# Kernel optimization log

Hardware: AMD Instinct MI355X
Metric: run time of the kernel (lower is better)

## Reference

```python
import jax, jax.numpy as jnp
import numpy as np

B, D_IN, D_HID, NH, PF = 1024, 2048, 4096, 8, 2
D_UP = D_IN * PF          # 4096
HS = D_HID // NH          # 512 head size
EPS = 1e-5


def setup_inputs() -> dict:
    key = jax.random.key(0)
    ks = jax.random.split(key, 24)
    it = iter(range(24))

    def lin(k, fin, fout):
        # weight stored as (in, out); y = x @ W + b
        return jax.random.normal(k, (fin, fout), jnp.float32) / np.float32(np.sqrt(fin))

    def bd(k, fin_blk, fout_blk):
        # block-diagonal per-head weights (NH, in_blk, out_blk)
        return jax.random.normal(k, (NH, fin_blk, fout_blk), jnp.float32) / np.float32(np.sqrt(fin_blk))

    inp = {}
    inp['x'] = jax.random.normal(ks[next(it)], (B, D_IN), jnp.float32)
    inp['h_prev'] = jax.random.normal(ks[next(it)], (B, D_HID), jnp.float32)
    inp['c_prev'] = jax.random.normal(ks[next(it)], (B, D_HID), jnp.float32)
    inp['n_prev'] = jax.random.normal(ks[next(it)], (B, D_HID), jnp.float32)
    inp['m_prev'] = jax.random.normal(ks[next(it)], (B, D_HID), jnp.float32)
    inp['ln_w'] = jnp.ones((D_IN,), jnp.float32)
    inp['ln_b'] = jnp.zeros((D_IN,), jnp.float32)
    inp['upL_w'] = lin(ks[next(it)], D_IN, D_UP); inp['upL_b'] = jnp.zeros((D_UP,), jnp.float32)
    inp['upR_w'] = lin(ks[next(it)], D_IN, D_HID); inp['upR_b'] = jnp.zeros((D_HID,), jnp.float32)
    inp['conv_w'] = jax.random.normal(ks[next(it)], (1, 1, 4), jnp.float32) * 0.5  # (O,I,K)
    inp['conv_b'] = jnp.zeros((1,), jnp.float32)
    inp['skip_w'] = lin(ks[next(it)], D_UP, D_HID); inp['skip_b'] = jnp.zeros((D_HID,), jnp.float32)
    inp['wq'] = bd(ks[next(it)], D_UP // NH, HS); inp['bq'] = jnp.zeros((NH, HS), jnp.float32)
    inp['wk'] = bd(ks[next(it)], D_UP // NH, HS); inp['bk'] = jnp.zeros((NH, HS), jnp.float32)
    inp['wv'] = bd(ks[next(it)], D_UP // NH, HS); inp['bv'] = jnp.zeros((NH, HS), jnp.float32)
    inp['wi_w'] = lin(ks[next(it)], D_UP, D_HID); inp['wi_b'] = jnp.zeros((D_HID,), jnp.float32)
    inp['wf_w'] = lin(ks[next(it)], D_UP, D_HID); inp['wf_b'] = jnp.zeros((D_HID,), jnp.float32)
    inp['wo_w'] = lin(ks[next(it)], D_UP, D_HID); inp['wo_b'] = jnp.zeros((D_HID,), jnp.float32)
    inp['gn_w'] = jnp.ones((D_HID,), jnp.float32)
    inp['gn_b'] = jnp.zeros((D_HID,), jnp.float32)
    inp['down_w'] = lin(ks[next(it)], D_HID, D_IN); inp['down_b'] = jnp.zeros((D_IN,), jnp.float32)
    return inp


def _forward(x, h_prev, c_prev, n_prev, m_prev, ln_w, ln_b, upL_w, upL_b, upR_w, upR_b,
             conv_w, conv_b, skip_w, skip_b, wq, bq, wk, bk, wv, bv,
             wi_w, wi_b, wf_w, wf_b, wo_w, wo_b, gn_w, gn_b, down_w, down_b):
    b = x.shape[0]
    # LayerNorm(input_size)
    mu = jnp.mean(x, axis=-1, keepdims=True)
    var = jnp.var(x, axis=-1, keepdims=True)
    x_norm = (x - mu) * jax.lax.rsqrt(var + EPS) * ln_w + ln_b

    x_up_left = x_norm @ upL_w + upL_b     # (B, D_UP)
    x_up_right = x_norm @ upR_w + upR_b    # (B, D_HID)

    # CausalConv1D(1,1,4): left-pad 3, valid conv  == torch pad 3 both sides + drop last 3
    conv = jax.lax.conv_general_dilated(
        x_up_left[:, None, :], conv_w, window_strides=(1,), padding=((3, 0),),
        dimension_numbers=('NCH', 'OIH', 'NCH'))
    x_conv = jax.nn.silu(conv[:, 0, :] + conv_b[0])   # (B, D_UP)

    x_skip = x_conv @ skip_w + skip_b                 # (B, D_HID)

    def blockdiag(xv, w, bias):
        xh = xv.reshape(b, NH, -1)                    # (B, NH, in_blk)
        return (jnp.einsum('bhi,hio->bho', xh, w) + bias).reshape(b, -1)

    q = blockdiag(x_conv, wq, bq)                                  # (B, D_HID)
    k = blockdiag(x_conv, wk, bk) / np.float32(np.sqrt(HS))
    v = blockdiag(x_up_left, wv, bv)

    i_tilde = x_conv @ wi_w + wi_b
    f_tilde = x_conv @ wf_w + wf_b
    o = jax.nn.sigmoid(x_up_left @ wo_w + wo_b)

    # stabilized exponential gating
    m_t = jnp.maximum(f_tilde + m_prev, i_tilde)
    i_g = jnp.exp(i_tilde - m_t)
    f_g = jnp.exp(f_tilde + m_prev - m_t)
    c_t = f_g * c_prev + i_g * (v * k)
    n_t = f_g * n_prev + i_g * k

    # torch.max(torch.abs(n_t.T @ q), 1)[0] -> (D_HID,)
    denom = jnp.max(jnp.abs(n_t.T @ q), axis=1)
    h_t = o * (c_t * q) / denom                       # broadcast (B,D_HID)/(D_HID,)

    # GroupNorm(NH, D_HID) on 2D input
    hg = h_t.reshape(b, NH, HS)
    mu_g = jnp.mean(hg, axis=-1, keepdims=True)
    var_g = jnp.var(hg, axis=-1, keepdims=True)
    gn = ((hg - mu_g) * jax.lax.rsqrt(var_g + EPS)).reshape(b, D_HID) * gn_w + gn_b

    out = (gn + x_skip) * jax.nn.silu(x_up_right)
    final = out @ down_w + down_b + x
    return final, h_t, c_t, n_t, m_t


def reference(x, h_prev, c_prev, n_prev, m_prev, ln_w, ln_b, upL_w, upL_b, upR_w, upR_b,
              conv_w, conv_b, skip_w, skip_b, wq, bq, wk, bk, wv, bv,
              wi_w, wi_b, wf_w, wf_b, wo_w, wo_b, gn_w, gn_b, down_w, down_b):
    return _forward(x, h_prev, c_prev, n_prev, m_prev, ln_w, ln_b, upL_w, upL_b, upR_w, upR_b,
                    conv_w, conv_b, skip_w, skip_b, wq, bq, wk, bk, wv, bv,
                    wi_w, wi_b, wf_w, wf_b, wo_w, wo_b, gn_w, gn_b, down_w, down_b)
```

## Files before the change

### kernel.cpp

```cpp
#include <hip/hip_runtime.h>
#include <math.h>

#define B_ROWS 1024
#define D_IN   2048
#define D_HID  4096
#define D_UP   4096
#define NH     8
#define HS     512
#define LN_EPS 1e-5f

typedef __attribute__((ext_vector_type(8))) short bf16x8_t;
typedef __attribute__((ext_vector_type(4))) float f32x4_t;
typedef __attribute__((ext_vector_type(4))) unsigned short us4_t;

__device__ __forceinline__ unsigned short f2bf(float f) {
    unsigned int u = __float_as_uint(f);
    u += 0x7fffu + ((u >> 16) & 1u);
    return (unsigned short)(u >> 16);
}
__device__ __forceinline__ float bf2f(unsigned short u) {
    return __uint_as_float(((unsigned int)u) << 16);
}
__device__ __forceinline__ float sigmoidf_(float x) { return 1.0f / (1.0f + expf(-x)); }
__device__ __forceinline__ float siluf_(float x)    { return x / (1.0f + expf(-x)); }

__device__ __forceinline__ void gload16(const unsigned short* g, unsigned short* l) {
    __builtin_amdgcn_global_load_lds(
        (const __attribute__((address_space(1))) unsigned int*)(const void*)g,
        (__attribute__((address_space(3))) unsigned int*)(void*)l,
        16, 0, 0);
}

#define VMW(n) asm volatile("s_waitcnt vmcnt(" #n ")" ::: "memory")

#define XCD_SWZ()                                                        \
    int bx = blockIdx.x, by = blockIdx.y;                                \
    {                                                                    \
        const int gx_ = gridDim.x;                                       \
        const int n_  = gx_ * gridDim.y;                                 \
        if ((n_ & 7) == 0) {                                             \
            int lin = by * gx_ + bx;                                     \
            const int q8 = n_ >> 3;                                      \
            lin = (lin & 7) * q8 + (lin >> 3);                           \
            bx = lin % gx_; by = lin / gx_;                              \
        }                                                                \
    }

struct MGChunk {
    const unsigned short* A;
    const unsigned short* Bt;
    const float* bias;
    const float* resid;
    float* C;
    unsigned short* C2;
    float* denom;
    float alpha;
    int epi;
};

template<int NCH>
__global__ __launch_bounds__(256, 2) void mg256(
    MGChunk c0, MGChunk c1, MGChunk c2, MGChunk c3,
    int K, int lda, int ldbt, int ldc, int bpc,
    long aB, long wB, long bB, long cB)
{
    const int gx = gridDim.x, gy = gridDim.y;
    const int n = gx * gy;
    const int orig = blockIdx.y * gx + blockIdx.x;
    const int wl = ((n & 7) == 0) ? ((orig & 7) * (n >> 3) + (orig >> 3)) : orig;
    const int bxw = wl / gy;
    const int byw = wl - bxw * gy;
    const int chid = (NCH > 1) ? (bxw / bpc) : 0;
    const int cbx = bxw - chid * bpc;
    const MGChunk ch = (chid == 0) ? c0 : ((chid == 1) ? c1 : ((chid == 2) ? c2 : c3));
    const int bz = blockIdx.z;

    const unsigned short* A  = ch.A  + bz * aB;
    const unsigned short* Bt = ch.Bt + bz * wB;

    __shared__ __align__(16) unsigned short As[3][256][32];
    __shared__ __align__(16) unsigned short Bs[3][128][32];

    const int t = threadIdx.x;
    const int w = t >> 6, l = t & 63;
    const int wrm = w >> 1;
    const int wcn = w & 1;
    const long rowA = (long)byw * 256;
    const long rowB = (long)cbx * 128;

    const int skz = (((l & 3) ^ ((l >> 3) & 3)) << 3);
    const unsigned short* Ag = A  + rowA * (long)lda;
    const unsigned short* Bg = Bt + rowB * (long)ldbt;

    const int lm  = l & 15;
    const int pkz = (((l >> 4) ^ ((l >> 1) & 3)) << 3);

    f32x4_t acc[8][4];
#pragma unroll
    for (int mi = 0; mi < 8; ++mi)
#pragma unroll
        for (int ni = 0; ni < 4; ++ni) acc[mi][ni] = (f32x4_t)0.0f;

#define STAGE(buf, kb)                                                        \
    {                                                                         \
        _Pragma("unroll")                                                     \
        for (int p = 0; p < 4; ++p)                                           \
            gload16(Ag + (long)(w * 64 + p * 16 + (l >> 2)) * lda + (kb) + skz, \
                    &As[buf][w * 64 + p * 16][0]);                            \
        _Pragma("unroll")                                                     \
        for (int p = 0; p < 2; ++p)                                           \
            gload16(Bg + (long)(w * 32 + p * 16 + (l >> 2)) * ldbt + (kb) + skz, \
                    &Bs[buf][w * 32 + p * 16][0]);                            \
    }

    const int nsteps = K >> 5;
    STAGE(0, 0);
    STAGE(1, 32);

    int cur = 0;
    for (int ti = 0; ti < nsteps; ++ti) {
        int nxt2 = cur + 2; if (nxt2 >= 3) nxt2 -= 3;
        if (ti + 2 < nsteps) {
            STAGE(nxt2, (ti + 2) << 5);
            VMW(12);
        } else if (ti + 2 == nsteps) {
            VMW(6);
        } else {
            VMW(0);
        }
        __builtin_amdgcn_s_barrier();

        bf16x8_t bfr[4];
#pragma unroll
        for (int ni = 0; ni < 4; ++ni)
            bfr[ni] = *(const bf16x8_t*)&Bs[cur][wcn * 64 + ni * 16 + lm][pkz];
#pragma unroll
        for (int mi = 0; mi < 8; ++mi) {
            const bf16x8_t af = *(const bf16x8_t*)&As[cur][wrm * 128 + mi * 16 + lm][pkz];
#pragma unroll
            for (int ni = 0; ni < 4; ++ni)
                acc[mi][ni] = __builtin_amdgcn_mfma_f32_16x16x32_bf16(
                    af, bfr[ni], acc[mi][ni], 0, 0, 0);
        }

        asm volatile("s_waitcnt lgkmcnt(0)" ::: "memory");
        __builtin_amdgcn_s_barrier();
        cur = (cur == 2) ? 0 : cur + 1;
    }
#undef STAGE

    const int lr4 = (l >> 4) * 4;
    if (ch.epi == 3) {
        float rmax[8][4];
#pragma unroll
        for (int mi = 0; mi < 8; ++mi)
#pragma unroll
            for (int r = 0; r < 4; ++r) {
                float m = 0.0f;
#pragma unroll
                for (int ni = 0; ni < 4; ++ni) m = fmaxf(m, fabsf(acc[mi][ni][r]));
                rmax[mi][r] = m;
            }
#pragma unroll
        for (int off = 1; off < 16; off <<= 1)
#pragma unroll
            for (int mi = 0; mi < 8; ++mi)
#pragma unroll
                for (int r = 0; r < 4; ++r)
                    rmax[mi][r] = fmaxf(rmax[mi][r], __shfl_xor(rmax[mi][r], off, 64));
        if (lm == 0) {
#pragma unroll
            for (int mi = 0; mi < 8; ++mi)
#pragma unroll
                for (int r = 0; r < 4; ++r) {
                    const long m = rowA + wrm * 128 + mi * 16 + lr4 + r;
                    atomicMax((unsigned int*)&ch.denom[m], __float_as_uint(rmax[mi][r]));
                }
        }
        return;
    }
    const float* bias = ch.bias + bz * bB;
#pragma unroll
    for (int mi = 0; mi < 8; ++mi) {
        const long m0 = rowA + wrm * 128 + mi * 16 + lr4;
#pragma unroll
        for (int ni = 0; ni < 4; ++ni) {
            const long nn = rowB + wcn * 64 + ni * 16 + lm;
            const float bv = bias[nn];
#pragma unroll
            for (int r = 0; r < 4; ++r) {
                float v = acc[mi][ni][r] + bv;
                if (ch.epi == 2) v *= ch.alpha;
                const long m = m0 + r;
                if (ch.epi == 5) (ch.C2 + bz * cB)[m * ldc + nn] = f2bf(v);
                else             (ch.C  + bz * cB)[m * ldc + nn] = v;
            }
        }
    }
}

struct MCChunk {
    const unsigned short* A;
    const unsigned short* Bt;
    const float* bias;
    float* C;
    unsigned short* C2;
    float alpha;
    int epi;
};

template<int NCH>
__global__ __launch_bounds__(256) void mgemm_mc(
    MCChunk c0, MCChunk c1, MCChunk c2,
    int K, int lda, int ldbt, int ldc, int bpc,
    long aB, long wB, long bB, long cB)
{
    XCD_SWZ();
    const int chid = bx / bpc;
    const int cbx  = bx - chid * bpc;
    const MCChunk ch = (chid == 0) ? c0 : ((NCH > 1 && chid == 1) ? c1 : c2);
    const int bz = blockIdx.z;

    const unsigned short* A  = ch.A  + bz * aB;
    const unsigned short* Bt = ch.Bt + bz * wB;
    const float* bias = ch.bias + bz * bB;

    __shared__ __align__(16) unsigned short As[2][128][40];
    __shared__ __align__(16) unsigned short Bs[2][128][40];

    const int t = threadIdx.x;
    const int w = t >> 6, l = t & 63;
    const int wr = w >> 1, wc = w & 1;
    const long rowA = (long)by * 128;
    const long rowB = (long)cbx * 128;

    const int lr = t >> 2;
    const int lc = (t & 3) << 3;
    const unsigned short* Ag = A  + (rowA + lr) * (long)lda  + lc;
    const unsigned short* Bg = Bt + (rowB + lr) * (long)ldbt + lc;

    const int lm = l & 15;
    const int lk = (l >> 4) * 8;

    f32x4_t acc[4][4];
#pragma unroll
    for (int mi = 0; mi < 4; ++mi)
#pragma unroll
        for (int ni = 0; ni < 4; ++ni) acc[mi][ni] = (f32x4_t)0.0f;

    bf16x8_t ra[2], rb[2];
#pragma unroll
    for (int p = 0; p < 2; ++p) {
        ra[p] = *(const bf16x8_t*)(Ag + (long)p * 64 * lda);
        rb[p] = *(const bf16x8_t*)(Bg + (long)p * 64 * ldbt);
    }
#pragma unroll
    for (int p = 0; p < 2; ++p) {
        *(bf16x8_t*)&As[0][lr + p * 64][lc] = ra[p];
        *(bf16x8_t*)&Bs[0][lr + p * 64][lc] = rb[p];
    }
    __syncthreads();

    const int nsteps = K >> 5;
    for (int ti = 0; ti < nsteps; ++ti) {
        const int cur = ti & 1;
        if (ti + 1 < nsteps) {
            const int kb = (ti + 1) << 5;
#pragma unroll
            for (int p = 0; p < 2; ++p) {
                ra[p] = *(const bf16x8_t*)(Ag + (long)p * 64 * lda  + kb);
                rb[p] = *(const bf16x8_t*)(Bg + (long)p * 64 * ldbt + kb);
            }
        }
        bf16x8_t af[4], bfr[4];
#pragma unroll
        for (int mi = 0; mi < 4; ++mi)
            af[mi] = *(const bf16x8_t*)&As[cur][wr * 64 + mi * 16 + lm][lk];
#pragma unroll
        for (int ni = 0; ni < 4; ++ni)
            bfr[ni] = *(const bf16x8_t*)&Bs[cur][wc * 64 + ni * 16 + lm][lk];
#pragma unroll
        for (int mi = 0; mi < 4; ++mi)
#pragma unroll
            for (int ni = 0; ni < 4; ++ni)
                acc[mi][ni] = __builtin_amdgcn_mfma_f32_16x16x32_bf16(
                    af[mi], bfr[ni], acc[mi][ni], 0, 0, 0);
        if (ti + 1 < nsteps) {
            const int nxt = cur ^ 1;
#pragma unroll
            for (int p = 0; p < 2; ++p) {
                *(bf16x8_t*)&As[nxt][lr + p * 64][lc] = ra[p];
                *(bf16x8_t*)&Bs[nxt][lr + p * 64][lc] = rb[p];
            }
        }
        __syncthreads();
    }

    const int lr4 = (l >> 4) * 4;
    const float alpha = ch.alpha;
#pragma unroll
    for (int mi = 0; mi < 4; ++mi) {
        const long m0 = rowA + wr * 64 + mi * 16 + lr4;
#pragma unroll
        for (int ni = 0; ni < 4; ++ni) {
            const long nn = rowB + wc * 64 + ni * 16 + lm;
            const float bv = bias[nn];
#pragma unroll
            for (int r = 0; r < 4; ++r) {
                const float v = (acc[mi][ni][r] + bv) * alpha;
                const long m = m0 + r;
                if (ch.epi == 5) (ch.C2 + bz * cB)[m * ldc + nn] = f2bf(v);
                else             (ch.C  + bz * cB)[m * ldc + nn] = v;
            }
        }
    }
}

template<int BM, int EPI>
__global__ __launch_bounds__(256) void mgemm(
    const unsigned short* __restrict__ A, const unsigned short* __restrict__ Bt,
    const float* __restrict__ bias, const float* __restrict__ resid,
    float* __restrict__ C, float* __restrict__ denom,
    int K, int lda, int ldbt, int ldc)
{
    constexpr int MR = BM / 32;
    constexpr int AP = BM / 64;
    XCD_SWZ();

    __shared__ __align__(16) unsigned short As[2][BM][40];
    __shared__ __align__(16) unsigned short Bs[2][128][40];

    const int t = threadIdx.x;
    const int w = t >> 6, l = t & 63;
    const int wr = w >> 1, wc = w & 1;
    const long rowA = (long)by * BM;
    const long rowB = (long)bx * 128;

    const int lr = t >> 2;
    const int lc = (t & 3) << 3;
    const unsigned short* Ag = A  + (rowA + lr) * (long)lda  + lc;
    const unsigned short* Bg = Bt + (rowB + lr) * (long)ldbt + lc;

    const int lm = l & 15;
    const int lk = (l >> 4) * 8;

    f32x4_t acc[MR][4];
#pragma unroll
    for (int mi = 0; mi < MR; ++mi)
#pragma unroll
        for (int ni = 0; ni < 4; ++ni) acc[mi][ni] = (f32x4_t)0.0f;

    bf16x8_t ra[AP], rb[2];
#pragma unroll
    for (int p = 0; p < AP; ++p) ra[p] = *(const bf16x8_t*)(Ag + (long)p * 64 * lda);
#pragma unroll
    for (int p = 0; p < 2;  ++p) rb[p] = *(const bf16x8_t*)(Bg + (long)p * 64 * ldbt);
#pragma unroll
    for (int p = 0; p < AP; ++p) *(bf16x8_t*)&As[0][lr + p * 64][lc] = ra[p];
#pragma unroll
    for (int p = 0; p < 2;  ++p) *(bf16x8_t*)&Bs[0][lr + p * 64][lc] = rb[p];
    __syncthreads();

    const int nsteps = K >> 5;
    for (int ti = 0; ti < nsteps; ++ti) {
        const int cur = ti & 1;
        if (ti + 1 < nsteps) {
            const int kb = (ti + 1) << 5;
#pragma unroll
            for (int p = 0; p < AP; ++p) ra[p] = *(const bf16x8_t*)(Ag + (long)p * 64 * lda  + kb);
#pragma unroll
            for (int p = 0; p < 2;  ++p) rb[p] = *(const bf16x8_t*)(Bg + (long)p * 64 * ldbt + kb);
        }
        bf16x8_t af[MR], bfr[4];
#pragma unroll
        for (int mi = 0; mi < MR; ++mi)
            af[mi] = *(const bf16x8_t*)&As[cur][wr * (BM / 2) + mi * 16 + lm][lk];
#pragma unroll
        for (int ni = 0; ni < 4; ++ni)
            bfr[ni] = *(const bf16x8_t*)&Bs[cur][wc * 64 + ni * 16 + lm][lk];
#pragma unroll
        for (int mi = 0; mi < MR; ++mi)
#pragma unroll
            for (int ni = 0; ni < 4; ++ni)
                acc[mi][ni] = __builtin_amdgcn_mfma_f32_16x16x32_bf16(
                    af[mi], bfr[ni], acc[mi][ni], 0, 0, 0);
        if (ti + 1 < nsteps) {
            const int nxt = cur ^ 1;
#pragma unroll
            for (int p = 0; p < AP; ++p) *(bf16x8_t*)&As[nxt][lr + p * 64][lc] = ra[p];
#pragma unroll
            for (int p = 0; p < 2;  ++p) *(bf16x8_t*)&Bs[nxt][lr + p * 64][lc] = rb[p];
        }
        __syncthreads();
    }

    const int lr4 = (l >> 4) * 4;
#pragma unroll
    for (int mi = 0; mi < MR; ++mi) {
        const long m0 = rowA + wr * (BM / 2) + mi * 16 + lr4;
#pragma unroll
        for (int ni = 0; ni < 4; ++ni) {
            const long nn = rowB + wc * 64 + ni * 16 + lm;
            const float bv = bias[nn];
#pragma unroll
            for (int r = 0; r < 4; ++r) {
                float v = acc[mi][ni][r] + bv;
                const long m = m0 + r;
                if (EPI == 4) v += resid[m * ldc + nn];
                C[m * ldc + nn] = v;
            }
        }
    }
}

struct TP4 {
    const float* s0; const float* s1; const float* s2; const float* s3;
    unsigned short* d0; unsigned short* d1; unsigned short* d2; unsigned short* d3;
};

__global__ __launch_bounds__(256) void tp_batch(TP4 tp, int R, int C)
{
    const int z = blockIdx.z;
    const float* X = (z == 0) ? tp.s0 : (z == 1) ? tp.s1 : (z == 2) ? tp.s2 : tp.s3;
    unsigned short* XT = (z == 0) ? tp.d0 : (z == 1) ? tp.d1 : (z == 2) ? tp.d2 : tp.d3;
    __shared__ float tile[64][65];
    const int t = threadIdx.x;
    const long r0 = (long)blockIdx.y * 64;
    const long c0 = (long)blockIdx.x * 64;
    const int tr = t >> 4;
    const int tc = (t & 15) << 2;
#pragma unroll
    for (int p = 0; p < 4; ++p) {
        const float4 v = *(const float4*)(X + (r0 + tr + p * 16) * C + c0 + tc);
        tile[tr + p * 16][tc + 0] = v.x;
        tile[tr + p * 16][tc + 1] = v.y;
        tile[tr + p * 16][tc + 2] = v.z;
        tile[tr + p * 16][tc + 3] = v.w;
    }
    __syncthreads();
#pragma unroll
    for (int p = 0; p < 4; ++p) {
        const int cc = tr + p * 16;
        us4_t o;
        o.x = f2bf(tile[tc + 0][cc]);
        o.y = f2bf(tile[tc + 1][cc]);
        o.z = f2bf(tile[tc + 2][cc]);
        o.w = f2bf(tile[tc + 3][cc]);
        *(us4_t*)(XT + (c0 + cc) * (long)R + r0 + tc) = o;
    }
}

__global__ __launch_bounds__(256) void tp_qkv(
    const float* wq, const float* wk, const float* wv, unsigned short* dst)
{
    const int z = blockIdx.z;
    const int sel = z >> 3, head = z & 7;
    const float* X = ((sel == 0) ? wq : (sel == 1) ? wk : wv) + (long)head * HS * HS;
    unsigned short* XT = dst + (long)sel * NH * HS * HS + (long)head * HS * HS;
    __shared__ float tile[64][65];
    const int t = threadIdx.x;
    const long r0 = (long)blockIdx.y * 64;
    const long c0 = (long)blockIdx.x * 64;
    const int tr = t >> 4;
    const int tc = (t & 15) << 2;
#pragma unroll
    for (int p = 0; p < 4; ++p) {
        const float4 v = *(const float4*)(X + (r0 + tr + p * 16) * HS + c0 + tc);
        tile[tr + p * 16][tc + 0] = v.x;
        tile[tr + p * 16][tc + 1] = v.y;
        tile[tr + p * 16][tc + 2] = v.z;
        tile[tr + p * 16][tc + 3] = v.w;
    }
    __syncthreads();
#pragma unroll
    for (int p = 0; p < 4; ++p) {
        const int cc = tr + p * 16;
        us4_t o;
        o.x = f2bf(tile[tc + 0][cc]);
        o.y = f2bf(tile[tc + 1][cc]);
        o.z = f2bf(tile[tc + 2][cc]);
        o.w = f2bf(tile[tc + 3][cc]);
        *(us4_t*)(XT + (c0 + cc) * (long)HS + r0 + tc) = o;
    }
}

__global__ __launch_bounds__(256) void layernorm_kernel(
    const float* __restrict__ x, const float* __restrict__ w,
    const float* __restrict__ b, unsigned short* __restrict__ out)
{
    __shared__ float sh[8];
    const int row = blockIdx.x, t = threadIdx.x;
    const float* xr = x + (long)row * D_IN;
    float v[8];
    float s = 0.f, ss = 0.f;
#pragma unroll
    for (int i = 0; i < 8; ++i) {
        v[i] = xr[t + 256 * i];
        s += v[i];
        ss += v[i] * v[i];
    }
#pragma unroll
    for (int off = 32; off; off >>= 1) {
        s  += __shfl_down(s, off, 64);
        ss += __shfl_down(ss, off, 64);
    }
    const int lane = t & 63, wid = t >> 6;
    if (lane == 0) { sh[wid * 2] = s; sh[wid * 2 + 1] = ss; }
    __syncthreads();
    s = 0.f; ss = 0.f;
#pragma unroll
    for (int i = 0; i < 4; ++i) { s += sh[i * 2]; ss += sh[i * 2 + 1]; }
    const float mu  = s * (1.0f / D_IN);
    const float var = ss * (1.0f / D_IN) - mu * mu;
    const float rs  = rsqrtf(var + LN_EPS);
    unsigned short* orow = out + (long)row * D_IN;
#pragma unroll
    for (int i = 0; i < 8; ++i) {
        const int d = t + 256 * i;
        orow[d] = f2bf((v[i] - mu) * rs * w[d] + b[d]);
    }
}

__global__ void conv_silu_kernel(const unsigned short* __restrict__ xl,
                                 const float* __restrict__ cw,
                                 const float* __restrict__ cb,
                                 unsigned short* __restrict__ out)
{
    const long idx = (long)blockIdx.x * blockDim.x + threadIdx.x;
    if (idx >= (long)B_ROWS * D_UP) return;
    const int d = (int)(idx & (D_UP - 1));
    const float w0 = cw[0], w1 = cw[1], w2 = cw[2], w3 = cw[3];
    float acc = cb[0] + w3 * bf2f(xl[idx]);
    if (d >= 1) acc += w2 * bf2f(xl[idx - 1]);
    if (d >= 2) acc += w1 * bf2f(xl[idx - 2]);
    if (d >= 3) acc += w0 * bf2f(xl[idx - 3]);
    out[idx] = f2bf(siluf_(acc));
}

__global__ void gating_kernel(const float* __restrict__ it, const float* __restrict__ ft,
                              const float* __restrict__ mp, const float* __restrict__ cp,
                              const float* __restrict__ np_, const float* __restrict__ kk,
                              const float* __restrict__ vv,
                              float* __restrict__ mt, float* __restrict__ ct,
                              float* __restrict__ nt)
{
    const long idx = (long)blockIdx.x * blockDim.x + threadIdx.x;
    if (idx >= (long)B_ROWS * D_HID) return;
    const float i_t = it[idx];
    const float f_t = ft[idx] + mp[idx];
    const float m_t = fmaxf(f_t, i_t);
    const float i_g = expf(i_t - m_t);
    const float f_g = expf(f_t - m_t);
    const float kv  = kk[idx];
    ct[idx] = f_g * cp[idx] + i_g * (vv[idx] * kv);
    nt[idx] = f_g * np_[idx] + i_g * kv;
    mt[idx] = m_t;
}

__global__ __launch_bounds__(128) void hgnorm_kernel(
    const unsigned short* __restrict__ op, const float* __restrict__ ct,
    const float* __restrict__ qb, const float* __restrict__ denom,
    const float* __restrict__ gw, const float* __restrict__ gb,
    const unsigned short* __restrict__ xskip, const unsigned short* __restrict__ xupR,
    float* __restrict__ ht, unsigned short* __restrict__ out)
{
    __shared__ float sh[4];
    const int b = blockIdx.x >> 3, h = blockIdx.x & 7;
    const int t = threadIdx.x;
    const long base = (long)b * D_HID + h * HS;
    float v[4];
    float s = 0.f, ss = 0.f;
#pragma unroll
    for (int i = 0; i < 4; ++i) {
        const long ix = base + t + 128 * i;
        const int  dg = h * HS + t + 128 * i;
        const float hv = sigmoidf_(bf2f(op[ix])) * ct[ix] * qb[ix] / denom[dg];
        ht[ix] = hv;
        v[i] = hv;
        s += hv;
        ss += hv * hv;
    }
#pragma unroll
    for (int off = 32; off; off >>= 1) {
        s  += __shfl_down(s, off, 64);
        ss += __shfl_down(ss, off, 64);
    }
    if ((t & 63) == 0) { sh[(t >> 6) * 2] = s; sh[(t >> 6) * 2 + 1] = ss; }
    __syncthreads();
    s = sh[0] + sh[2];
    ss = sh[1] + sh[3];
    const float mu  = s * (1.0f / HS);
    const float var = ss * (1.0f / HS) - mu * mu;
    const float rs  = rsqrtf(var + LN_EPS);
#pragma unroll
    for (int i = 0; i < 4; ++i) {
        const int  dg = h * HS + t + 128 * i;
        const long ix = base + t + 128 * i;
        const float g = (v[i] - mu) * rs * gw[dg] + gb[dg];
        out[ix] = f2bf((g + bf2f(xskip[ix])) * siluf_(bf2f(xupR[ix])));
    }
}

extern "C" void kernel_launch(void* const* d_in, const int* in_sizes, int n_in,
                              void* d_out, int out_size, void* d_ws, size_t ws_size,
                              hipStream_t stream)
{
    const float* x      = (const float*)d_in[0];
    const float* c_prev = (const float*)d_in[2];
    const float* n_prev = (const float*)d_in[3];
    const float* m_prev = (const float*)d_in[4];
    const float* ln_w   = (const float*)d_in[5];
    const float* ln_b   = (const float*)d_in[6];
    const float* upL_w  = (const float*)d_in[7];
    const float* upL_b  = (const float*)d_in[8];
    const float* upR_w  = (const float*)d_in[9];
    const float* upR_b  = (const float*)d_in[10];
    const float* conv_w = (const float*)d_in[11];
    const float* conv_b = (const float*)d_in[12];
    const float* skip_w = (const float*)d_in[13];
    const float* skip_b = (const float*)d_in[14];
    const float* wq     = (const float*)d_in[15];
    const float* bq     = (const float*)d_in[16];
    const float* wk     = (const float*)d_in[17];
    const float* bk     = (const float*)d_in[18];
    const float* wv     = (const float*)d_in[19];
    const float* bv     = (const float*)d_in[20];
    const float* wi_w   = (const float*)d_in[21];
    const float* wi_b   = (const float*)d_in[22];
    const float* wf_w   = (const float*)d_in[23];
    const float* wf_b   = (const float*)d_in[24];
    const float* wo_w   = (const float*)d_in[25];
    const float* wo_b   = (const float*)d_in[26];
    const float* gn_w   = (const float*)d_in[27];
    const float* gn_b   = (const float*)d_in[28];
    const float* down_w = (const float*)d_in[29];
    const float* down_b = (const float*)d_in[30];

    float* out     = (float*)d_out;
    float* final_o = out;
    float* ht      = final_o + 2097152;
    float* ct      = ht + 4194304;
    float* nt      = ct + 4194304;
    float* mt      = nt + 4194304;

    unsigned short* WTA = (unsigned short*)ht;
    unsigned short* WTB = (unsigned short*)nt;

    const long M = 1048576;
    float* ws = (float*)d_ws;
    float* qb  = ws +  0 * M;
    float* kb  = ws +  4 * M;
    float* vb  = ws +  8 * M;
    float* itb = ws + 12 * M;
    float* ftb = ws + 16 * M;
    unsigned short* xupR_bf  = (unsigned short*)(ws + 20 * M);
    unsigned short* xskip_bf = (unsigned short*)(ws + 22 * M);
    unsigned short* opb_bf   = (unsigned short*)(ws + 24 * M);
    unsigned short* xnorm_bf = (unsigned short*)(ws + 26 * M);
    unsigned short* xupL_bf  = (unsigned short*)(ws + 27 * M);
    unsigned short* xconv_bf = (unsigned short*)(ws + 29 * M);
    float* denom             = ws + 31 * M;
    unsigned short* WTC      = (unsigned short*)(ws + 32 * M);
    unsigned short* WTD      = (unsigned short*)(ws +  0 * M);
    unsigned short* ntT      = (unsigned short*)(ws + 26 * M);
    unsigned short* qT       = (unsigned short*)(ws + 28 * M);
    unsigned short* dwT      = (unsigned short*)(ws + 12 * M);
    unsigned short* tmp_bf   = (unsigned short*)(ws +  8 * M);

    const float kscale = 1.0f / sqrtf((float)HS);
    const long HS2 = (long)HS * HS;
    MGChunk cz = {};
    MCChunk mz = {};

    layernorm_kernel<<<B_ROWS, 256, 0, stream>>>(x, ln_w, ln_b, xnorm_bf);

    {
        TP4 tp = { upL_w, upR_w, nullptr, nullptr, WTA, WTA + 8388608, nullptr, nullptr };
        tp_batch<<<dim3(64, 32, 2), 256, 0, stream>>>(tp, D_IN, D_UP);
    }
    {
        MCChunk a = { xnorm_bf, WTA,           upL_b, nullptr, xupL_bf, 1.0f, 5 };
        MCChunk b = { xnorm_bf, WTA + 8388608, upR_b, nullptr, xupR_bf, 1.0f, 5 };
        mgemm_mc<2><<<dim3(64, 8, 1), 256, 0, stream>>>(
            a, b, mz, D_IN, D_IN, D_IN, D_HID, 32, 0, 0, 0, 0);
    }

    conv_silu_kernel<<<(B_ROWS * D_UP) / 256, 256, 0, stream>>>(xupL_bf, conv_w, conv_b, xconv_bf);

    {
        TP4 tp = { skip_w, wi_w, wf_w, wo_w, WTA, WTB, WTC, WTD };
        tp_batch<<<dim3(64, 64, 4), 256, 0, stream>>>(tp, D_UP, D_HID);
    }
    {
        MGChunk a = { xconv_bf, WTA, skip_b, nullptr, nullptr, xskip_bf, nullptr, 1.0f, 5 };
        MGChunk b = { xconv_bf, WTB, wi_b,   nullptr, itb,     nullptr,  nullptr, 1.0f, 0 };
        MGChunk c = { xconv_bf, WTC, wf_b,   nullptr, ftb,     nullptr,  nullptr, 1.0f, 0 };
        MGChunk d = { xupL_bf,  WTD, wo_b,   nullptr, nullptr, opb_bf,   nullptr, 1.0f, 5 };
        mg256<4><<<dim3(128, 4, 1), 256, 0, stream>>>(
            a, b, c, d, D_UP, D_UP, D_UP, D_HID, 32, 0, 0, 0, 0);
    }

    tp_qkv<<<dim3(8, 8, 24), 256, 0, stream>>>(wq, wk, wv, WTA);
    {
        MCChunk a = { xconv_bf, WTA,                bq, qb, nullptr, 1.0f,   0 };
        MCChunk b = { xconv_bf, WTA + NH * HS2,     bk, kb, nullptr, kscale, 0 };
        MCChunk c = { xupL_bf,  WTA + 2 * NH * HS2, bv, vb, nullptr, 1.0f,   0 };
        mgemm_mc<3><<<dim3(12, 8, NH), 256, 0, stream>>>(
            a, b, c, HS, D_UP, HS, D_HID, 4, HS, HS2, HS, HS);
    }

    gating_kernel<<<(B_ROWS * D_HID) / 256, 256, 0, stream>>>(
        itb, ftb, m_prev, c_prev, n_prev, kb, vb, mt, ct, nt);

    {
        TP4 tp = { nt, qb, nullptr, nullptr, ntT, qT, nullptr, nullptr };
        tp_batch<<<dim3(64, 16, 2), 256, 0, stream>>>(tp, B_ROWS, D_HID);
    }
    hipMemsetAsync(denom, 0, D_HID * sizeof(float), stream);
    {
        MGChunk a = { ntT, qT, nullptr, nullptr, nullptr, nullptr, denom, 1.0f, 3 };
        mg256<1><<<dim3(32, 16, 1), 256, 0, stream>>>(
            a, cz, cz, cz, B_ROWS, B_ROWS, B_ROWS, 0, 32, 0, 0, 0, 0);
    }

    {
        TP4 tp = { down_w, nullptr, nullptr, nullptr, dwT, nullptr, nullptr, nullptr };
        tp_batch<<<dim3(32, 64, 1), 256, 0, stream>>>(tp, D_HID, D_IN);
    }

    hgnorm_kernel<<<B_ROWS * NH, 128, 0, stream>>>(
        opb_bf, ct, qb, denom, gn_w, gn_b, xskip_bf, xupR_bf, ht, tmp_bf);

    mgemm<64, 4><<<dim3(16, 16, 1), 256, 0, stream>>>(
        tmp_bf, dwT, down_b, x, final_o, nullptr, D_HID, D_HID, D_HID, D_IN);
}
```

Measured before the change: 561.7 us.

## Interleave global prefetch slices with MFMA phases and raise wave priority

Splits each K-step of the GEMM main loop into four phases. Each phase issues one slice of the next-next tile's global-to-LDS loads, then runs two rows of MFMAs wrapped in s_setprio, with extra barriers between phases. The goal is to spread memory issue across the compute so load latency overlaps better with matrix math and waves stay in step. In exchange it adds three barriers per K-step and moves the vmcnt wait to the end of the iteration, which could add synchronisation stalls.

```diff
diff --git a/kernel.cpp b/kernel.cpp
--- a/kernel.cpp
+++ b/kernel.cpp
@@ -113,41 +113,69 @@
                     &Bs[buf][w * 32 + p * 16][0]);                            \
     }
 
+#define SLICE_AB(p_)                                                          \
+    if (pf) {                                                                 \
+        gload16(Ag + (long)(w * 64 + (p_) * 16 + (l >> 2)) * lda + kb2 + skz, \
+                &As[nxt2][w * 64 + (p_) * 16][0]);                            \
+        if ((p_) < 2)                                                         \
+            gload16(Bg + (long)(w * 32 + (p_) * 16 + (l >> 2)) * ldbt + kb2 + skz, \
+                    &Bs[nxt2][w * 32 + (p_) * 16][0]);                        \
+    }
+
+#define APHASE(q)                                                             \
+    {                                                                         \
+        const bf16x8_t a0 = *(const bf16x8_t*)&As[cur][wrm * 128 + (2*(q)) * 16 + lm][pkz]; \
+        const bf16x8_t a1 = *(const bf16x8_t*)&As[cur][wrm * 128 + (2*(q)+1) * 16 + lm][pkz]; \
+        __builtin_amdgcn_s_setprio(1);                                        \
+        _Pragma("unroll")                                                     \
+        for (int ni = 0; ni < 4; ++ni)                                        \
+            acc[2*(q)][ni] = __builtin_amdgcn_mfma_f32_16x16x32_bf16(         \
+                a0, bfr[ni], acc[2*(q)][ni], 0, 0, 0);                        \
+        _Pragma("unroll")                                                     \
+        for (int ni = 0; ni < 4; ++ni)                                        \
+            acc[2*(q)+1][ni] = __builtin_amdgcn_mfma_f32_16x16x32_bf16(       \
+                a1, bfr[ni], acc[2*(q)+1][ni], 0, 0, 0);                      \
+        __builtin_amdgcn_s_setprio(0);                                        \
+    }
+
     const int nsteps = K >> 5;
     STAGE(0, 0);
     STAGE(1, 32);
+    VMW(6);
+    __builtin_amdgcn_s_barrier();
 
     int cur = 0;
     for (int ti = 0; ti < nsteps; ++ti) {
         int nxt2 = cur + 2; if (nxt2 >= 3) nxt2 -= 3;
-        if (ti + 2 < nsteps) {
-            STAGE(nxt2, (ti + 2) << 5);
-            VMW(12);
-        } else if (ti + 2 == nsteps) {
-            VMW(6);
-        } else {
-            VMW(0);
-        }
-        __builtin_amdgcn_s_barrier();
+        const bool pf = (ti + 2 < nsteps);
+        const int kb2 = (ti + 2) << 5;
 
         bf16x8_t bfr[4];
+        SLICE_AB(0)
 #pragma unroll
         for (int ni = 0; ni < 4; ++ni)
             bfr[ni] = *(const bf16x8_t*)&Bs[cur][wcn * 64 + ni * 16 + lm][pkz];
-#pragma unroll
-        for (int mi = 0; mi < 8; ++mi) {
-            const bf16x8_t af = *(const bf16x8_t*)&As[cur][wrm * 128 + mi * 16 + lm][pkz];
-#pragma unroll
-            for (int ni = 0; ni < 4; ++ni)
-                acc[mi][ni] = __builtin_amdgcn_mfma_f32_16x16x32_bf16(
-                    af, bfr[ni], acc[mi][ni], 0, 0, 0);
-        }
-
+        APHASE(0)
+        __builtin_amdgcn_s_barrier();
+
+        SLICE_AB(1)
+        APHASE(1)
+        __builtin_amdgcn_s_barrier();
+
+        SLICE_AB(2)
+        APHASE(2)
+        __builtin_amdgcn_s_barrier();
+
+        SLICE_AB(3)
+        APHASE(3)
+        if (pf) { VMW(6); } else { VMW(0); }
         asm volatile("s_waitcnt lgkmcnt(0)" ::: "memory");
         __builtin_amdgcn_s_barrier();
         cur = (cur == 2) ? 0 : cur + 1;
     }
 #undef STAGE
+#undef SLICE_AB
+#undef APHASE
 
     const int lr4 = (l >> 4) * 4;
     if (ch.epi == 3) {
```

New measurement: 679.6 us. 21.0% more time.
